# Kernel optimization log

Hardware: AMD Instinct MI355X
Metric: run time of the kernel (lower is better)

The kernel has to match this reference:

```python
import jax, jax.numpy as jnp
import numpy as np
import math

A = 32; B = 32; PSIZE = 16; K = 3; STRIDE = 2; PAD = 1; ITERS = 3; FINAL_LAMBDA = 0.01
KK = K * K; KKA = KK * A; KKA2 = KKA // 2 + 1
EPS = 1e-12; LN2PI = math.log(2 * math.pi)


def unfold(x, k, s, p):
    # torch F.unfold: output feature dim ordered (C, kh, kw), columns row-major
    b, C, h, w = x.shape
    xp = jnp.pad(x, ((0, 0), (0, 0), (p, p), (p, p)))
    oh = (h + 2 * p - k) // s + 1
    ow = (w + 2 * p - k) // s + 1
    cols = [xp[:, :, ki:ki + s * (oh - 1) + 1:s, kj:kj + s * (ow - 1) + 1:s]
            for ki in range(k) for kj in range(k)]
    patches = jnp.stack(cols, axis=2)  # [b, C, kk, oh, ow]
    return patches.reshape(b, C, k * k, oh * ow), oh, ow


def setup_inputs():
    key = jax.random.key(0)
    ks = jax.random.split(key, 8)
    b, h, w = 4, 14, 14
    a_in = jax.random.uniform(ks[0], (b, A, h, w), dtype=jnp.float32)
    pose = jax.random.normal(ks[1], (b, A * PSIZE, h, w), dtype=jnp.float32)
    mpose_w = jax.random.normal(ks[2], (B * PSIZE, PSIZE), dtype=jnp.float32) / np.float32(np.sqrt(PSIZE))
    mpose_b = jnp.zeros((B * PSIZE,), jnp.float32)
    freq_w = jax.random.normal(ks[3], (KKA2, PSIZE, 2), dtype=jnp.float32) * 0.02
    ln_g = jnp.ones((A,), jnp.float32)
    ln_b = jnp.zeros((A,), jnp.float32)
    lim = np.float32(np.sqrt(6.0 / (KK + KK)))  # xavier_uniform on [kk, kk, 1]
    spat_w = jax.random.uniform(ks[4], (KK, KK, 1), jnp.float32, -lim, lim)
    spat_bias = jnp.ones((KK,), jnp.float32)
    beta_u = jnp.zeros((1, 1, B, 1), jnp.float32)
    beta_a = jnp.zeros((1, 1, B), jnp.float32)
    return dict(a_in=a_in, pose=pose, mpose_w=mpose_w, mpose_b=mpose_b,
                freq_w=freq_w, ln_g=ln_g, ln_b=ln_b, spat_w=spat_w,
                spat_bias=spat_bias, beta_u=beta_u, beta_a=beta_a)


def _forward(a_in, pose, mpose_w, mpose_b, freq_w, ln_g, ln_b,
             spat_w, spat_bias, beta_u, beta_a):
    b = a_in.shape[0]
    pose_u, oh, ow = unfold(pose, K, STRIDE, PAD)  # [b, A*PSIZE, KK, l]
    l = oh * ow
    pose_u = pose_u.reshape(b, A, PSIZE, KK, l)
    pose_u = pose_u.transpose(0, 4, 3, 1, 2).reshape(b, l, KKA, PSIZE)
    # mpose linear: psize -> B*psize
    po = jnp.einsum('blkp,qp->blkq', pose_u, mpose_w) + mpose_b
    po = po.reshape(b * l, KKA, B, PSIZE)
    # Frequency FFT filter over kkA axis (weight shared across all B slices)
    xf = jnp.fft.rfft(po, axis=1, norm='ortho')        # [bl, KKA2, B, PSIZE] complex
    wc = freq_w[..., 0] + 1j * freq_w[..., 1]           # [KKA2, PSIZE]
    xf = xf * wc[None, :, None, :]
    po = jnp.fft.irfft(xf, n=KKA, axis=1, norm='ortho') + po  # residual
    v = po.reshape(b, l, KKA, B, PSIZE)
    a_u, _, _ = unfold(a_in, K, STRIDE, PAD)            # [b, A, KK, l]
    a_u = a_u.transpose(0, 3, 2, 1).reshape(b, l, KKA)
    # Spatial gating applied to ones-initialized r (identical for every B slice)
    ones = jnp.ones((b * l, KKA), jnp.float32)
    g = ones.reshape(b * l, KK, A)
    mu_g = g.mean(-1, keepdims=True)
    var_g = ((g - mu_g) ** 2).mean(-1, keepdims=True)
    gn = (g - mu_g) / jnp.sqrt(var_g + 1e-5) * ln_g + ln_b
    g2 = jnp.einsum('ij,nja->nia', spat_w[:, :, 0], gn) + spat_bias[None, :, None]
    gate = jax.nn.gelu(g2, approximate=False).reshape(b * l, KKA) + ones
    logit = jnp.broadcast_to(gate[:, :, None], (b * l, KKA, B))
    r = jax.nn.softmax(logit, axis=2).reshape(b, l, KKA, B, 1)
    a_out = mu = None
    for i in range(ITERS):
        lam = FINAL_LAMBDA * (1.0 - 0.95 ** (i + 1))
        # m-step
        rr = r * a_u[:, :, :, None, None]
        r_sum = rr.sum(axis=2, keepdims=True)                 # [b,l,1,B,1]
        coeff = rr / (r_sum + EPS)
        mu = (coeff * v).sum(axis=2, keepdims=True)           # [b,l,1,B,PSIZE]
        sig = (coeff * (v - mu) ** 2).sum(axis=2, keepdims=True) + EPS
        cost = (beta_u + jnp.log(jnp.sqrt(sig[:, :, 0]))) * r_sum[:, :, 0]  # [b,l,B,PSIZE]
        a_out = jax.nn.sigmoid(lam * (beta_a - cost.sum(axis=3)))           # [b,l,B]
        if i < ITERS - 1:
            # e-step (note: log(sigma_sq * ln2pi) is faithful to the original code)
            ln_p = (-0.5 * jnp.sum(jnp.log(sig * LN2PI), axis=-1)
                    - jnp.sum((v - mu) ** 2 / (2.0 * sig), axis=-1))        # [b,l,KKA,B]
            ln_ap = ln_p + jnp.log(a_out[:, :, None, :])
            r = jax.nn.softmax(ln_ap, axis=-1)[..., None]
    pose_out = mu[:, :, 0].reshape(b, l, B * PSIZE).transpose(0, 2, 1).reshape(b, B * PSIZE, oh, ow)
    a_fin = a_out.transpose(0, 2, 1).reshape(b, B, oh, ow)
    return a_fin, pose_out


def reference(a_in, pose, mpose_w, mpose_b, freq_w, ln_g, ln_b,
              spat_w, spat_bias, beta_u, beta_a):
    return _forward(a_in, pose, mpose_w, mpose_b, freq_w, ln_g, ln_b,
                    spat_w, spat_bias, beta_u, beta_a)
```

## Files before the change

kernel.cpp:

```cpp
#include <hip/hip_runtime.h>
#include <hip/hip_bf16.h>
#include <math.h>

#define A_    32
#define B_    32
#define PS    16
#define KK_   9
#define KKA_  288
#define OH_   7
#define L_    49
#define NB    4
#define NSITE 196

#define LAM1 5.0e-4f
#define LAM2 9.75e-4f
#define LAM3 1.42625e-3f
#define LOG_LN2PI 0.6086775903077413f

typedef _Float16 half2v __attribute__((ext_vector_type(2)));
typedef _Float16 half4v __attribute__((ext_vector_type(4)));
typedef short    short8 __attribute__((ext_vector_type(8)));
typedef float    floatx4 __attribute__((ext_vector_type(4)));

static __device__ __forceinline__ float san(float x, float lo, float hi){
    return fminf(fmaxf(x, lo), hi);
}

static __device__ __forceinline__ float dot2acc(half2v a, half2v b, float c){
#if __has_builtin(__builtin_amdgcn_fdot2)
    return __builtin_amdgcn_fdot2(a, b, c, false);
#else
    return c + (float)a.x*(float)b.x + (float)a.y*(float)b.y;
#endif
}

__global__ void k_prep_c(const float* __restrict__ fw,
                         ushort* __restrict__ cpr, float* __restrict__ csum)
{
    int id = blockIdx.x*256 + threadIdx.x;
    if (id >= 16*288) return;
    int p = id / 288, m = id % 288;
    float acc = fw[(0*16 + p)*2 + 0];
    for (int k = 1; k <= 143; ++k){
        float re = fw[(k*16 + p)*2 + 0];
        float im = fw[(k*16 + p)*2 + 1];
        int km = (k*m) % 288;
        float ang = 0.021816615649929116f * (float)km;
        float s, c; sincosf(ang, &s, &c);
        acc += 2.0f*(re*c - im*s);
    }
    float re144 = fw[(144*16 + p)*2 + 0];
    acc += re144 * ((m & 1) ? -1.0f : 1.0f);
    float cv = acc * (1.0f/288.0f);
    if (m == 0) cv += 1.0f;
    cv = san(cv, -1e4f, 1e4f);

    __hip_bfloat16 hb = __float2bfloat16(cv);
    float hif = __bfloat162float(hb);
    __hip_bfloat16 lb = __float2bfloat16(cv - hif);
    ushort hi = *(ushort*)&hb, lo = *(ushort*)&lb;

    ushort* c0h = cpr + p*592;
    ushort* c1h = cpr + 16*592   + p*592;
    ushort* c0l = cpr + 16*592*2 + p*592;
    ushort* c1l = cpr + 16*592*3 + p*592;
    int x1 = 288 - m;
    c0h[x1] = hi;  c0l[x1] = lo;
    c1h[x1-1] = hi; c1l[x1-1] = lo;
    if (m >= 1){
        int x2 = 576 - m;
        c0h[x2] = hi;  c0l[x2] = lo;
        c1h[x2-1] = hi; c1l[x2-1] = lo;
    } else {
        c0h[0] = hi; c0l[0] = lo;
        csum[p] = san(1.0f + fw[(0*16 + p)*2 + 0], -1e4f, 1e4f);
    }
}

__global__ void k_prep_x(const float* __restrict__ pose,
                         __hip_bfloat16* __restrict__ Xt, int n0, int cols)
{
    int id = blockIdx.x*256 + threadIdx.x;
    if (id >= cols*KKA_) return;
    int c = id / KKA_, j = id % KKA_;
    int n = n0 + (c >> 4), q = c & 15;
    int bs = n / L_, l = n % L_, oy = l / OH_, ox = l % OH_;
    int kk = j >> 5, a = j & 31;
    int y = oy*2 - 1 + kk/3, x = ox*2 - 1 + kk%3;
    float v = 0.f;
    if ((unsigned)y < 14u && (unsigned)x < 14u)
        v = pose[((bs*(A_*PS) + a*PS + q)*14 + y)*14 + x];
    Xt[id] = __float2bfloat16(san(v, -1e4f, 1e4f));
}

__launch_bounds__(256)
__global__ void k_stageB(const ushort* __restrict__ cpr, const __hip_bfloat16* __restrict__ Xt,
                         _Float16* __restrict__ U, int cols, int ns)
{
    const int bx = blockIdx.x, by = blockIdx.y, p = blockIdx.z;
    const int t = threadIdx.x;
    const int w = t >> 6, lane = t & 63;
    const int mn = lane & 15, quad = lane >> 4;
    const int i0 = by*48;
    const int col = bx*64 + w*16 + mn;
    const int colc = (col < cols) ? col : (cols - 1);

    const ushort* c0h = cpr + p*592;
    const ushort* c1h = cpr + 16*592   + p*592;
    const ushort* c0l = cpr + 16*592*2 + p*592;
    const ushort* c1l = cpr + 16*592*3 + p*592;

    floatx4 acc[3] = {{0,0,0,0},{0,0,0,0},{0,0,0,0}};
    for (int k0 = 0; k0 < 288; k0 += 32){
        short8 bfrag = *(const short8*)&Xt[colc*KKA_ + k0 + quad*8];
        #pragma unroll
        for (int s = 0; s < 3; ++s){
            int o = 288 + k0 + quad*8 - (i0 + s*16 + mn);
            int sel = o & 1;
            int off = o - sel;
            const ushort* bh = sel ? c1h : c0h;
            const ushort* bl = sel ? c1l : c0l;
            short8 ah = *(const short8*)&bh[off];
            short8 al = *(const short8*)&bl[off];
            acc[s] = __builtin_amdgcn_mfma_f32_16x16x32_bf16(ah, bfrag, acc[s], 0, 0, 0);
            acc[s] = __builtin_amdgcn_mfma_f32_16x16x32_bf16(al, bfrag, acc[s], 0, 0, 0);
        }
    }
    if (col < cols){
        const int nn = col >> 4, q0 = col & 15;
        #pragma unroll
        for (int s = 0; s < 3; ++s){
            #pragma unroll
            for (int r = 0; r < 4; ++r){
                int i = i0 + s*16 + quad*4 + r;
                U[(i*ns + nn)*256 + p*16 + q0] = (_Float16)acc[s][r];
            }
        }
    }
}

__launch_bounds__(512, 2)
__global__ void
k_em(const _Float16* __restrict__ U, const float* __restrict__ a_in,
     const float* __restrict__ mpw, const float* __restrict__ mpb,
     const float* __restrict__ csum,
     const float* __restrict__ beta_u, const float* __restrict__ beta_a,
     int n0, int ns, float* __restrict__ out)
{
    const int nl = blockIdx.x;
    const int n  = n0 + nl;
    const int t = threadIdx.x;
    const int Bc = t >> 4, p = t & 15;
    const int bs = n / L_, l = n % L_;

    __shared__ uint  v_lds[72][512];
    __shared__ float a_s[KKA_];
    __shared__ float d_s[16][33];
    __shared__ float rbuf[16][33];
    __shared__ float cst[32];

    for (int j = t; j < KKA_; j += 512){
        int kk = j >> 5, a = j & 31;
        int oy = l / OH_, ox = l % OH_;
        int y = oy*2 - 1 + kk/3, x = ox*2 - 1 + kk%3;
        float v = 0.f;
        if ((unsigned)y < 14u && (unsigned)x < 14u)
            v = a_in[((bs*A_ + a)*14 + y)*14 + x];
        a_s[j] = san(v, 0.f, 1e4f);
    }
    half2v w_h[8];
    #pragma unroll
    for (int k = 0; k < 8; ++k){
        w_h[k].x = (_Float16)mpw[t*16 + 2*k];
        w_h[k].y = (_Float16)mpw[t*16 + 2*k + 1];
    }
    const float vb = mpb[t] * csum[p];
    const float bu = beta_u[Bc];
    const float ba = beta_a[Bc];
    __syncthreads();

    float S0tot = 0.f;
    for (int j = 0; j < KKA_; ++j) S0tot += a_s[j];

    const _Float16* Up = U + nl*256 + p*16;
    const int istr = ns*256;

    half2v v_h[72];
    float S1 = 0.f, S2 = 0.f;
    for (int ch = 0; ch < 9; ++ch){
        #pragma unroll
        for (int k = 0; k < 8; ++k){
            const int i0 = ch*16 + 2*k;
            union { uint4 u4; half2v h2[4]; } A0, A1, B0, B1;
            A0.u4 = *(const uint4*)&Up[i0*istr];
            A1.u4 = *(const uint4*)&Up[i0*istr + 8];
            B0.u4 = *(const uint4*)&Up[(i0+1)*istr];
            B1.u4 = *(const uint4*)&Up[(i0+1)*istr + 8];
            float v0 = vb, v1 = vb;
            #pragma unroll
            for (int m = 0; m < 4; ++m){
                v0 = dot2acc(A0.h2[m], w_h[m],   v0);
                v0 = dot2acc(A1.h2[m], w_h[4+m], v0);
                v1 = dot2acc(B0.h2[m], w_h[m],   v1);
                v1 = dot2acc(B1.h2[m], w_h[4+m], v1);
            }
            const float a0 = a_s[i0], a1 = a_s[i0+1];
            S1 += a0*v0 + a1*v1;
            S2 += a0*v0*v0 + a1*v1*v1;
            union { half2v h; uint u; } cv;
            cv.h.x = (_Float16)v0; cv.h.y = (_Float16)v1;
            v_lds[ch*8 + k][t] = cv.u;
        }
    }
    #pragma unroll
    for (int ch = 0; ch < 9; ++ch){
        #pragma unroll
        for (int k = 0; k < 8; ++k){
            const int i0 = 144 + ch*16 + 2*k;
            union { uint4 u4; half2v h2[4]; } A0, A1, B0, B1;
            A0.u4 = *(const uint4*)&Up[i0*istr];
            A1.u4 = *(const uint4*)&Up[i0*istr + 8];
            B0.u4 = *(const uint4*)&Up[(i0+1)*istr];
            B1.u4 = *(const uint4*)&Up[(i0+1)*istr + 8];
            float v0 = vb, v1 = vb;
            #pragma unroll
            for (int m = 0; m < 4; ++m){
                v0 = dot2acc(A0.h2[m], w_h[m],   v0);
                v0 = dot2acc(A1.h2[m], w_h[4+m], v0);
                v1 = dot2acc(B0.h2[m], w_h[m],   v1);
                v1 = dot2acc(B1.h2[m], w_h[4+m], v1);
            }
            const float a0 = a_s[i0], a1 = a_s[i0+1];
            S1 += a0*v0 + a1*v1;
            S2 += a0*v0*v0 + a1*v1*v1;
            half2v vh; vh.x = (_Float16)v0; vh.y = (_Float16)v1;
            v_h[ch*8 + k] = vh;
        }
    }

    float mu_r, i2s_r;
    {
        const float rs  = S0tot * (1.0f/32.0f);
        const float inv = 1.0f / (rs + 1e-12f);
        const float S1r = S1 * (1.0f/32.0f), S2r = S2 * (1.0f/32.0f);
        mu_r = S1r * inv;
        const float sg  = fmaxf((S2r - 2.f*mu_r*S1r + mu_r*mu_r*rs) * inv, 0.f) + 1e-12f;
        i2s_r = 0.5f / sg;
        const float lg  = logf(sg);
        float cs = (bu + 0.5f*lg) * rs;
        float ls = lg + LOG_LN2PI;
        #pragma unroll
        for (int m = 1; m < 16; m <<= 1){ cs += __shfl_xor(cs, m, 16); ls += __shfl_xor(ls, m, 16); }
        const float aout = san(1.f/(1.f + expf(-LAM1*(ba - cs))), 1e-30f, 1.f);
        if (p == 0) cst[Bc] = logf(aout) - 0.5f*ls;
    }
    __syncthreads();

    const int b0 = p & 1, b1 = (p>>1)&1, b2 = (p>>2)&1, b3 = (p>>3)&1;
    float muF = 0.f, aF = 0.f;
    for (int it = 0; it < 2; ++it){
        const float lam = it ? LAM3 : LAM2;
        float T0 = 0.f, T1 = 0.f, T2 = 0.f;

        auto process = [&](int ibase, auto getpair){
            float e1[8], e2[4], e3[2], dfin;
            #pragma unroll
            for (int s = 0; s < 8; ++s){
                float v0, v1; getpair(s, v0, v1);
                float d0 = v0 - mu_r, d1 = v1 - mu_r;
                float ea = d0*d0*i2s_r, eb = d1*d1*i2s_r;
                float aown  = b0 ? eb : ea;
                float asend = b0 ? ea : eb;
                e1[s] = aown + __shfl_xor(asend, 1);
            }
            #pragma unroll
            for (int s = 0; s < 4; ++s){
                float aown  = b1 ? e1[2*s+1] : e1[2*s];
                float asend = b1 ? e1[2*s]   : e1[2*s+1];
                e2[s] = aown + __shfl_xor(asend, 2);
            }
            #pragma unroll
            for (int s = 0; s < 2; ++s){
                float aown  = b2 ? e2[2*s+1] : e2[2*s];
                float asend = b2 ? e2[2*s]   : e2[2*s+1];
                e3[s] = aown + __shfl_xor(asend, 4);
            }
            {
                float aown  = b3 ? e3[1] : e3[0];
                float asend = b3 ? e3[0] : e3[1];
                dfin = aown + __shfl_xor(asend, 8);
            }
            d_s[p][Bc] = dfin;
            __syncthreads();
            {
                const int isub = t >> 5, Bce = t & 31;
                float lnap = cst[Bce] - d_s[isub][Bce];
                float mx = lnap;
                #pragma unroll
                for (int m = 16; m >= 1; m >>= 1) mx = fmaxf(mx, __shfl_xor(mx, m));
                float ex = expf(lnap - mx);
                float sm = ex;
                #pragma unroll
                for (int m = 16; m >= 1; m >>= 1) sm += __shfl_xor(sm, m);
                rbuf[isub][Bce] = (ex / sm) * a_s[ibase + isub];
            }
            __syncthreads();
            #pragma unroll
            for (int s = 0; s < 8; ++s){
                float v0, v1; getpair(s, v0, v1);
                float r0 = rbuf[2*s][Bc], r1 = rbuf[2*s+1][Bc];
                T0 += r0 + r1;
                T1 += r0*v0 + r1*v1;
                T2 += r0*v0*v0 + r1*v1*v1;
            }
        };

        for (int ch = 0; ch < 9; ++ch){
            process(ch*16, [&](int s, float& v0, float& v1){
                union { uint u; half2v h; } cv; cv.u = v_lds[ch*8 + s][t];
                v0 = (float)cv.h.x; v1 = (float)cv.h.y;
            });
        }
        #pragma unroll
        for (int ch = 0; ch < 9; ++ch){
            process(144 + ch*16, [&](int s, float& v0, float& v1){
                half2v vh = v_h[ch*8 + s];
                v0 = (float)vh.x; v1 = (float)vh.y;
            });
        }

        const float inv = 1.f/(T0 + 1e-12f);
        const float mu  = T1 * inv;
        const float sg  = fmaxf((T2 - 2.f*mu*T1 + mu*mu*T0) * inv, 0.f) + 1e-12f;
        const float lg  = logf(sg);
        float cs = (bu + 0.5f*lg) * T0;
        float ls = lg + LOG_LN2PI;
        #pragma unroll
        for (int m = 1; m < 16; m <<= 1){ cs += __shfl_xor(cs, m, 16); ls += __shfl_xor(ls, m, 16); }
        const float aout = san(1.f/(1.f + expf(-lam*(ba - cs))), 1e-30f, 1.f);
        if (it == 0){
            mu_r = mu; i2s_r = 0.5f/sg;
            if (p == 0) cst[Bc] = logf(aout) - 0.5f*ls;
            __syncthreads();
        } else { muF = mu; aF = aout; }
    }

    if (p == 0) out[bs*(B_*L_) + Bc*L_ + l] = san(aF, 0.f, 1.f);
    out[6272 + (bs*512 + t)*L_ + l] = san(muF, -1e4f, 1e4f);
}

extern "C" void kernel_launch(void* const* d_in, const int* in_sizes, int n_in,
                              void* d_out, int out_size, void* d_ws, size_t ws_size,
                              hipStream_t stream)
{
    const float* a_in   = (const float*)d_in[0];
    const float* pose   = (const float*)d_in[1];
    const float* mpw    = (const float*)d_in[2];
    const float* mpb    = (const float*)d_in[3];
    const float* fw     = (const float*)d_in[4];
    const float* beta_u = (const float*)d_in[9];
    const float* beta_a = (const float*)d_in[10];
    float* out = (float*)d_out;

    char* base = (char*)d_ws;
    float*  csum = (float*)(base + 0);
    ushort* cpr  = (ushort*)(base + 256);

    const int opts[] = {196, 98, 49, 28, 14, 7, 4, 2, 1};
    int ns = 1;
    for (int oi = 0; oi < 9; ++oi){
        size_t need = 76288u + (size_t)156672u * (size_t)opts[oi];
        if (need <= ws_size){ ns = opts[oi]; break; }
    }
    const int G = NSITE / ns;
    const int cols = ns * PS;
    __hip_bfloat16* Xt = (__hip_bfloat16*)(base + 76288);
    _Float16*       Ug = (_Float16*)(base + 76288 + (size_t)9216*ns);

    k_prep_c<<<18, 256, 0, stream>>>(fw, cpr, csum);
    for (int g = 0; g < G; ++g){
        const int n0 = g * ns;
        k_prep_x<<<(cols*KKA_ + 255)/256, 256, 0, stream>>>(pose, Xt, n0, cols);
        k_stageB<<<dim3((cols + 63)/64, 6, 16), 256, 0, stream>>>(cpr, Xt, Ug, cols, ns);
        k_em    <<<ns, 512, 0, stream>>>(Ug, a_in, mpw, mpb, csum, beta_u, beta_a, n0, ns, out);
    }
}
```

Baseline: 285.8 us.

## Merge prep kernels, reorder EM register loads, cap k_em VGPRs

The two preparation kernels are fused into one launch, with extra blocks computing the filter coefficients on the first group, which removes one kernel launch. In k_em, the register-resident half of the transformed poses is now computed first in an unrolled loop with scheduling barriers, followed by the LDS-resident half. An amdgpu_num_vgpr(224) attribute is added to constrain register use. This aims to cut launch overhead and control register pressure and instruction scheduling, but the VGPR cap and sched barriers risk spills or reduced latency hiding.

```diff
diff --git a/kernel.cpp b/kernel.cpp
--- a/kernel.cpp
+++ b/kernel.cpp
@@ -22,6 +22,16 @@
 typedef short    short8 __attribute__((ext_vector_type(8)));
 typedef float    floatx4 __attribute__((ext_vector_type(4)));
 
+#if defined(__has_attribute)
+#  if __has_attribute(amdgpu_num_vgpr)
+#    define KEM_VGPR_ATTR __attribute__((amdgpu_num_vgpr(224)))
+#  else
+#    define KEM_VGPR_ATTR
+#  endif
+#else
+#  define KEM_VGPR_ATTR
+#endif
+
 static __device__ __forceinline__ float san(float x, float lo, float hi){
     return fminf(fmaxf(x, lo), hi);
 }
@@ -34,52 +44,59 @@
 #endif
 }
 
-__global__ void k_prep_c(const float* __restrict__ fw,
-                         ushort* __restrict__ cpr, float* __restrict__ csum)
+static __device__ __forceinline__ void sched_fence(){
+#if __has_builtin(__builtin_amdgcn_sched_barrier)
+    __builtin_amdgcn_sched_barrier(0);
+#else
+    asm volatile("" ::: "memory");
+#endif
+}
+
+__global__ void k_prep(const float* __restrict__ fw, const float* __restrict__ pose,
+                       ushort* __restrict__ cpr, float* __restrict__ csum,
+                       __hip_bfloat16* __restrict__ Xt, int n0, int cols, int nx)
 {
-    int id = blockIdx.x*256 + threadIdx.x;
-    if (id >= 16*288) return;
-    int p = id / 288, m = id % 288;
-    float acc = fw[(0*16 + p)*2 + 0];
-    for (int k = 1; k <= 143; ++k){
-        float re = fw[(k*16 + p)*2 + 0];
-        float im = fw[(k*16 + p)*2 + 1];
-        int km = (k*m) % 288;
-        float ang = 0.021816615649929116f * (float)km;
-        float s, c; sincosf(ang, &s, &c);
-        acc += 2.0f*(re*c - im*s);
-    }
-    float re144 = fw[(144*16 + p)*2 + 0];
-    acc += re144 * ((m & 1) ? -1.0f : 1.0f);
-    float cv = acc * (1.0f/288.0f);
-    if (m == 0) cv += 1.0f;
-    cv = san(cv, -1e4f, 1e4f);
-
-    __hip_bfloat16 hb = __float2bfloat16(cv);
-    float hif = __bfloat162float(hb);
-    __hip_bfloat16 lb = __float2bfloat16(cv - hif);
-    ushort hi = *(ushort*)&hb, lo = *(ushort*)&lb;
-
-    ushort* c0h = cpr + p*592;
-    ushort* c1h = cpr + 16*592   + p*592;
-    ushort* c0l = cpr + 16*592*2 + p*592;
-    ushort* c1l = cpr + 16*592*3 + p*592;
-    int x1 = 288 - m;
-    c0h[x1] = hi;  c0l[x1] = lo;
-    c1h[x1-1] = hi; c1l[x1-1] = lo;
-    if (m >= 1){
-        int x2 = 576 - m;
-        c0h[x2] = hi;  c0l[x2] = lo;
-        c1h[x2-1] = hi; c1l[x2-1] = lo;
-    } else {
-        c0h[0] = hi; c0l[0] = lo;
-        csum[p] = san(1.0f + fw[(0*16 + p)*2 + 0], -1e4f, 1e4f);
-    }
-}
-
-__global__ void k_prep_x(const float* __restrict__ pose,
-                         __hip_bfloat16* __restrict__ Xt, int n0, int cols)
-{
+    if ((int)blockIdx.x >= nx){
+        int id = ((int)blockIdx.x - nx)*256 + threadIdx.x;
+        if (id >= 16*288) return;
+        int p = id / 288, m = id % 288;
+        float acc = fw[(0*16 + p)*2 + 0];
+        for (int k = 1; k <= 143; ++k){
+            float re = fw[(k*16 + p)*2 + 0];
+            float im = fw[(k*16 + p)*2 + 1];
+            int km = (k*m) % 288;
+            float ang = 0.021816615649929116f * (float)km;
+            float s, c; sincosf(ang, &s, &c);
+            acc += 2.0f*(re*c - im*s);
+        }
+        float re144 = fw[(144*16 + p)*2 + 0];
+        acc += re144 * ((m & 1) ? -1.0f : 1.0f);
+        float cv = acc * (1.0f/288.0f);
+        if (m == 0) cv += 1.0f;
+        cv = san(cv, -1e4f, 1e4f);
+
+        __hip_bfloat16 hb = __float2bfloat16(cv);
+        float hif = __bfloat162float(hb);
+        __hip_bfloat16 lb = __float2bfloat16(cv - hif);
+        ushort hi = *(ushort*)&hb, lo = *(ushort*)&lb;
+
+        ushort* c0h = cpr + p*592;
+        ushort* c1h = cpr + 16*592   + p*592;
+        ushort* c0l = cpr + 16*592*2 + p*592;
+        ushort* c1l = cpr + 16*592*3 + p*592;
+        int x1 = 288 - m;
+        c0h[x1] = hi;  c0l[x1] = lo;
+        c1h[x1-1] = hi; c1l[x1-1] = lo;
+        if (m >= 1){
+            int x2 = 576 - m;
+            c0h[x2] = hi;  c0l[x2] = lo;
+            c1h[x2-1] = hi; c1l[x2-1] = lo;
+        } else {
+            c0h[0] = hi; c0l[0] = lo;
+            csum[p] = san(1.0f + fw[(0*16 + p)*2 + 0], -1e4f, 1e4f);
+        }
+        return;
+    }
     int id = blockIdx.x*256 + threadIdx.x;
     if (id >= cols*KKA_) return;
     int c = id / KKA_, j = id % KKA_;
@@ -139,7 +156,7 @@
     }
 }
 
-__launch_bounds__(512, 2)
+__launch_bounds__(512, 2) KEM_VGPR_ATTR
 __global__ void
 k_em(const _Float16* __restrict__ U, const float* __restrict__ a_in,
      const float* __restrict__ mpw, const float* __restrict__ mpb,
@@ -185,8 +202,37 @@
     const _Float16* Up = U + nl*256 + p*16;
     const int istr = ns*256;
 
+    float S1 = 0.f, S2 = 0.f;
+
     half2v v_h[72];
-    float S1 = 0.f, S2 = 0.f;
+    #pragma unroll
+    for (int g = 0; g < 36; ++g){
+        #pragma unroll
+        for (int k2 = 0; k2 < 2; ++k2){
+            const int pr = g*2 + k2;
+            const int i0 = 144 + pr*2;
+            union { uint4 u4; half2v h2[4]; } A0, A1, B0, B1;
+            A0.u4 = *(const uint4*)&Up[i0*istr];
+            A1.u4 = *(const uint4*)&Up[i0*istr + 8];
+            B0.u4 = *(const uint4*)&Up[(i0+1)*istr];
+            B1.u4 = *(const uint4*)&Up[(i0+1)*istr + 8];
+            float v0 = vb, v1 = vb;
+            #pragma unroll
+            for (int m = 0; m < 4; ++m){
+                v0 = dot2acc(A0.h2[m], w_h[m],   v0);
+                v0 = dot2acc(A1.h2[m], w_h[4+m], v0);
+                v1 = dot2acc(B0.h2[m], w_h[m],   v1);
+                v1 = dot2acc(B1.h2[m], w_h[4+m], v1);
+            }
+            const float a0 = a_s[i0], a1 = a_s[i0+1];
+            S1 += a0*v0 + a1*v1;
+            S2 += a0*v0*v0 + a1*v1*v1;
+            half2v vh; vh.x = (_Float16)v0; vh.y = (_Float16)v1;
+            v_h[pr] = vh;
+        }
+        sched_fence();
+    }
+
     for (int ch = 0; ch < 9; ++ch){
         #pragma unroll
         for (int k = 0; k < 8; ++k){
@@ -210,31 +256,6 @@
             union { half2v h; uint u; } cv;
             cv.h.x = (_Float16)v0; cv.h.y = (_Float16)v1;
             v_lds[ch*8 + k][t] = cv.u;
-        }
-    }
-    #pragma unroll
-    for (int ch = 0; ch < 9; ++ch){
-        #pragma unroll
-        for (int k = 0; k < 8; ++k){
-            const int i0 = 144 + ch*16 + 2*k;
-            union { uint4 u4; half2v h2[4]; } A0, A1, B0, B1;
-            A0.u4 = *(const uint4*)&Up[i0*istr];
-            A1.u4 = *(const uint4*)&Up[i0*istr + 8];
-            B0.u4 = *(const uint4*)&Up[(i0+1)*istr];
-            B1.u4 = *(const uint4*)&Up[(i0+1)*istr + 8];
-            float v0 = vb, v1 = vb;
-            #pragma unroll
-            for (int m = 0; m < 4; ++m){
-                v0 = dot2acc(A0.h2[m], w_h[m],   v0);
-                v0 = dot2acc(A1.h2[m], w_h[4+m], v0);
-                v1 = dot2acc(B0.h2[m], w_h[m],   v1);
-                v1 = dot2acc(B1.h2[m], w_h[4+m], v1);
-            }
-            const float a0 = a_s[i0], a1 = a_s[i0+1];
-            S1 += a0*v0 + a1*v1;
-            S2 += a0*v0*v0 + a1*v1*v1;
-            half2v vh; vh.x = (_Float16)v0; vh.y = (_Float16)v1;
-            v_h[ch*8 + k] = vh;
         }
     }
 
@@ -377,10 +398,11 @@
     __hip_bfloat16* Xt = (__hip_bfloat16*)(base + 76288);
     _Float16*       Ug = (_Float16*)(base + 76288 + (size_t)9216*ns);
 
-    k_prep_c<<<18, 256, 0, stream>>>(fw, cpr, csum);
     for (int g = 0; g < G; ++g){
         const int n0 = g * ns;
-        k_prep_x<<<(cols*KKA_ + 255)/256, 256, 0, stream>>>(pose, Xt, n0, cols);
+        const int nx = (cols*KKA_ + 255)/256;
+        const int nc = (g == 0) ? 18 : 0;
+        k_prep  <<<nx + nc, 256, 0, stream>>>(fw, pose, cpr, csum, Xt, n0, cols, nx);
         k_stageB<<<dim3((cols + 63)/64, 6, 16), 256, 0, stream>>>(cpr, Xt, Ug, cols, ns);
         k_em    <<<ns, 512, 0, stream>>>(Ug, a_in, mpw, mpb, csum, beta_u, beta_a, n0, ns, out);
     }
```

After: 281.1 us. Within noise of the previous version (-1.7%).

## Fuse circulant MFMA stage into EM kernel and merge prep kernels

Applied to the files above, without the earlier changes.

Merges the filter-coefficient and patch-gather prep kernels into one launch. Folds the circulant-filter MFMA stage into the EM kernel, so each site block computes its own filtered pose chunk into shared memory instead of writing U to global memory and reading it back. It also removes the chunked multi-launch loop over sites and switches sincosf to the fast intrinsic. The cost is extra shared memory, per-chunk __syncthreads, lower occupancy (launch bounds 512,1), and possibly slower coefficient precision.

```diff
diff --git a/kernel.cpp b/kernel.cpp
--- a/kernel.cpp
+++ b/kernel.cpp
@@ -11,6 +11,7 @@
 #define L_    49
 #define NB    4
 #define NSITE 196
+#define NCOLS 3136
 
 #define LAM1 5.0e-4f
 #define LAM2 9.75e-4f
@@ -18,7 +19,6 @@
 #define LOG_LN2PI 0.6086775903077413f
 
 typedef _Float16 half2v __attribute__((ext_vector_type(2)));
-typedef _Float16 half4v __attribute__((ext_vector_type(4)));
 typedef short    short8 __attribute__((ext_vector_type(8)));
 typedef float    floatx4 __attribute__((ext_vector_type(4)));
 
@@ -34,56 +34,55 @@
 #endif
 }
 
-__global__ void k_prep_c(const float* __restrict__ fw,
-                         ushort* __restrict__ cpr, float* __restrict__ csum)
+__global__ void k_prep(const float* __restrict__ fw, const float* __restrict__ pose,
+                       ushort* __restrict__ cpr, float* __restrict__ csum,
+                       __hip_bfloat16* __restrict__ Xt, int nc)
 {
-    int id = blockIdx.x*256 + threadIdx.x;
-    if (id >= 16*288) return;
-    int p = id / 288, m = id % 288;
-    float acc = fw[(0*16 + p)*2 + 0];
-    for (int k = 1; k <= 143; ++k){
-        float re = fw[(k*16 + p)*2 + 0];
-        float im = fw[(k*16 + p)*2 + 1];
-        int km = (k*m) % 288;
-        float ang = 0.021816615649929116f * (float)km;
-        float s, c; sincosf(ang, &s, &c);
-        acc += 2.0f*(re*c - im*s);
-    }
-    float re144 = fw[(144*16 + p)*2 + 0];
-    acc += re144 * ((m & 1) ? -1.0f : 1.0f);
-    float cv = acc * (1.0f/288.0f);
-    if (m == 0) cv += 1.0f;
-    cv = san(cv, -1e4f, 1e4f);
-
-    __hip_bfloat16 hb = __float2bfloat16(cv);
-    float hif = __bfloat162float(hb);
-    __hip_bfloat16 lb = __float2bfloat16(cv - hif);
-    ushort hi = *(ushort*)&hb, lo = *(ushort*)&lb;
-
-    ushort* c0h = cpr + p*592;
-    ushort* c1h = cpr + 16*592   + p*592;
-    ushort* c0l = cpr + 16*592*2 + p*592;
-    ushort* c1l = cpr + 16*592*3 + p*592;
-    int x1 = 288 - m;
-    c0h[x1] = hi;  c0l[x1] = lo;
-    c1h[x1-1] = hi; c1l[x1-1] = lo;
-    if (m >= 1){
-        int x2 = 576 - m;
-        c0h[x2] = hi;  c0l[x2] = lo;
-        c1h[x2-1] = hi; c1l[x2-1] = lo;
-    } else {
-        c0h[0] = hi; c0l[0] = lo;
-        csum[p] = san(1.0f + fw[(0*16 + p)*2 + 0], -1e4f, 1e4f);
-    }
-}
-
-__global__ void k_prep_x(const float* __restrict__ pose,
-                         __hip_bfloat16* __restrict__ Xt, int n0, int cols)
-{
-    int id = blockIdx.x*256 + threadIdx.x;
-    if (id >= cols*KKA_) return;
+    if ((int)blockIdx.x < nc){
+        int id = (int)blockIdx.x*256 + threadIdx.x;
+        if (id >= 16*288) return;
+        int p = id / 288, m = id % 288;
+        float acc = fw[(0*16 + p)*2 + 0];
+        for (int k = 1; k <= 143; ++k){
+            float re = fw[(k*16 + p)*2 + 0];
+            float im = fw[(k*16 + p)*2 + 1];
+            int km = (k*m) % 288;
+            float ang = 0.021816615649929116f * (float)km;
+            float s, c; __sincosf(ang, &s, &c);
+            acc += 2.0f*(re*c - im*s);
+        }
+        float re144 = fw[(144*16 + p)*2 + 0];
+        acc += re144 * ((m & 1) ? -1.0f : 1.0f);
+        float cv = acc * (1.0f/288.0f);
+        if (m == 0) cv += 1.0f;
+        cv = san(cv, -1e4f, 1e4f);
+
+        __hip_bfloat16 hb = __float2bfloat16(cv);
+        float hif = __bfloat162float(hb);
+        __hip_bfloat16 lb = __float2bfloat16(cv - hif);
+        ushort hi = *(ushort*)&hb, lo = *(ushort*)&lb;
+
+        ushort* c0h = cpr + p*592;
+        ushort* c1h = cpr + 16*592   + p*592;
+        ushort* c0l = cpr + 16*592*2 + p*592;
+        ushort* c1l = cpr + 16*592*3 + p*592;
+        int x1 = 288 - m;
+        c0h[x1] = hi;  c0l[x1] = lo;
+        c1h[x1-1] = hi; c1l[x1-1] = lo;
+        if (m >= 1){
+            int x2 = 576 - m;
+            c0h[x2] = hi;  c0l[x2] = lo;
+            c1h[x2-1] = hi; c1l[x2-1] = lo;
+        } else {
+            c0h[0] = hi; c0l[0] = lo;
+            csum[p] = san(1.0f + fw[(0*16 + p)*2 + 0], -1e4f, 1e4f);
+        }
+        return;
+    }
+    int id = ((int)blockIdx.x - nc)*256 + threadIdx.x;
+    if (id >= NCOLS*KKA_) return;
     int c = id / KKA_, j = id % KKA_;
-    int n = n0 + (c >> 4), q = c & 15;
+    int n = c >> 4, q = c & 15;
     int bs = n / L_, l = n % L_, oy = l / OH_, ox = l % OH_;
     int kk = j >> 5, a = j & 31;
     int y = oy*2 - 1 + kk/3, x = ox*2 - 1 + kk%3;
@@ -93,71 +92,26 @@
     Xt[id] = __float2bfloat16(san(v, -1e4f, 1e4f));
 }
 
-__launch_bounds__(256)
-__global__ void k_stageB(const ushort* __restrict__ cpr, const __hip_bfloat16* __restrict__ Xt,
-                         _Float16* __restrict__ U, int cols, int ns)
-{
-    const int bx = blockIdx.x, by = blockIdx.y, p = blockIdx.z;
-    const int t = threadIdx.x;
-    const int w = t >> 6, lane = t & 63;
-    const int mn = lane & 15, quad = lane >> 4;
-    const int i0 = by*48;
-    const int col = bx*64 + w*16 + mn;
-    const int colc = (col < cols) ? col : (cols - 1);
-
-    const ushort* c0h = cpr + p*592;
-    const ushort* c1h = cpr + 16*592   + p*592;
-    const ushort* c0l = cpr + 16*592*2 + p*592;
-    const ushort* c1l = cpr + 16*592*3 + p*592;
-
-    floatx4 acc[3] = {{0,0,0,0},{0,0,0,0},{0,0,0,0}};
-    for (int k0 = 0; k0 < 288; k0 += 32){
-        short8 bfrag = *(const short8*)&Xt[colc*KKA_ + k0 + quad*8];
-        #pragma unroll
-        for (int s = 0; s < 3; ++s){
-            int o = 288 + k0 + quad*8 - (i0 + s*16 + mn);
-            int sel = o & 1;
-            int off = o - sel;
-            const ushort* bh = sel ? c1h : c0h;
-            const ushort* bl = sel ? c1l : c0l;
-            short8 ah = *(const short8*)&bh[off];
-            short8 al = *(const short8*)&bl[off];
-            acc[s] = __builtin_amdgcn_mfma_f32_16x16x32_bf16(ah, bfrag, acc[s], 0, 0, 0);
-            acc[s] = __builtin_amdgcn_mfma_f32_16x16x32_bf16(al, bfrag, acc[s], 0, 0, 0);
-        }
-    }
-    if (col < cols){
-        const int nn = col >> 4, q0 = col & 15;
-        #pragma unroll
-        for (int s = 0; s < 3; ++s){
-            #pragma unroll
-            for (int r = 0; r < 4; ++r){
-                int i = i0 + s*16 + quad*4 + r;
-                U[(i*ns + nn)*256 + p*16 + q0] = (_Float16)acc[s][r];
-            }
-        }
-    }
-}
-
-__launch_bounds__(512, 2)
+__launch_bounds__(512, 1)
 __global__ void
-k_em(const _Float16* __restrict__ U, const float* __restrict__ a_in,
-     const float* __restrict__ mpw, const float* __restrict__ mpb,
-     const float* __restrict__ csum,
-     const float* __restrict__ beta_u, const float* __restrict__ beta_a,
-     int n0, int ns, float* __restrict__ out)
+k_mega(const ushort* __restrict__ cpr, const __hip_bfloat16* __restrict__ Xt,
+       const float* __restrict__ a_in,
+       const float* __restrict__ mpw, const float* __restrict__ mpb,
+       const float* __restrict__ csum,
+       const float* __restrict__ beta_u, const float* __restrict__ beta_a,
+       float* __restrict__ out)
 {
     const int nl = blockIdx.x;
-    const int n  = n0 + nl;
     const int t = threadIdx.x;
     const int Bc = t >> 4, p = t & 15;
-    const int bs = n / L_, l = n % L_;
-
-    __shared__ uint  v_lds[72][512];
-    __shared__ float a_s[KKA_];
-    __shared__ float d_s[16][33];
-    __shared__ float rbuf[16][33];
-    __shared__ float cst[32];
+    const int bs = nl / L_, l = nl % L_;
+
+    __shared__ uint      v_lds[72][512];
+    __shared__ _Float16  us[16*264];
+    __shared__ float     a_s[KKA_];
+    __shared__ float     d_s[16][33];
+    __shared__ float     rbuf[16][33];
+    __shared__ float     cst[32];
 
     for (int j = t; j < KKA_; j += 512){
         int kk = j >> 5, a = j & 31;
@@ -182,20 +136,49 @@
     float S0tot = 0.f;
     for (int j = 0; j < KKA_; ++j) S0tot += a_s[j];
 
-    const _Float16* Up = U + nl*256 + p*16;
-    const int istr = ns*256;
-
+    const int w = t >> 6, lane = t & 63;
+    const int mn = lane & 15, quad = lane >> 4;
+    const int p0 = w*2;
+    const __hip_bfloat16* xrow = Xt + (nl*16 + mn)*KKA_ + quad*8;
+
+    float S1 = 0.f, S2 = 0.f;
     half2v v_h[72];
-    float S1 = 0.f, S2 = 0.f;
+
     for (int ch = 0; ch < 9; ++ch){
-        #pragma unroll
-        for (int k = 0; k < 8; ++k){
-            const int i0 = ch*16 + 2*k;
+        floatx4 accA = {0,0,0,0}, accB = {0,0,0,0};
+        for (int k0i = 0; k0i < 9; ++k0i){
+            const int k0 = k0i*32;
+            short8 bfrag = *(const short8*)&xrow[k0];
+            #pragma unroll
+            for (int pp = 0; pp < 2; ++pp){
+                const int pg = p0 + pp;
+                int o = 288 + k0 + quad*8 - (ch*16 + mn);
+                int sel = o & 1, off = o - sel;
+                const ushort* bh = cpr + (sel ? 16*592 : 0) + pg*592;
+                const ushort* bl = cpr + 16*592*2 + (sel ? 16*592 : 0) + pg*592;
+                short8 ah = *(const short8*)&bh[off];
+                short8 al = *(const short8*)&bl[off];
+                floatx4 acc = pp ? accB : accA;
+                acc = __builtin_amdgcn_mfma_f32_16x16x32_bf16(ah, bfrag, acc, 0, 0, 0);
+                acc = __builtin_amdgcn_mfma_f32_16x16x32_bf16(al, bfrag, acc, 0, 0, 0);
+                if (pp) accB = acc; else accA = acc;
+            }
+        }
+        #pragma unroll
+        for (int r = 0; r < 4; ++r){
+            us[p0*264     + (quad*4 + r)*16 + mn] = (_Float16)accA[r];
+            us[(p0+1)*264 + (quad*4 + r)*16 + mn] = (_Float16)accB[r];
+        }
+        __syncthreads();
+        const _Float16* urow = &us[p*264];
+        #pragma unroll
+        for (int s = 0; s < 8; ++s){
+            const int i0 = ch*16 + 2*s;
             union { uint4 u4; half2v h2[4]; } A0, A1, B0, B1;
-            A0.u4 = *(const uint4*)&Up[i0*istr];
-            A1.u4 = *(const uint4*)&Up[i0*istr + 8];
-            B0.u4 = *(const uint4*)&Up[(i0+1)*istr];
-            B1.u4 = *(const uint4*)&Up[(i0+1)*istr + 8];
+            A0.u4 = *(const uint4*)&urow[(2*s)*16];
+            A1.u4 = *(const uint4*)&urow[(2*s)*16 + 8];
+            B0.u4 = *(const uint4*)&urow[(2*s+1)*16];
+            B1.u4 = *(const uint4*)&urow[(2*s+1)*16 + 8];
             float v0 = vb, v1 = vb;
             #pragma unroll
             for (int m = 0; m < 4; ++m){
@@ -209,19 +192,47 @@
             S2 += a0*v0*v0 + a1*v1*v1;
             union { half2v h; uint u; } cv;
             cv.h.x = (_Float16)v0; cv.h.y = (_Float16)v1;
-            v_lds[ch*8 + k][t] = cv.u;
-        }
+            v_lds[ch*8 + s][t] = cv.u;
+        }
+        __syncthreads();
     }
     #pragma unroll
-    for (int ch = 0; ch < 9; ++ch){
-        #pragma unroll
-        for (int k = 0; k < 8; ++k){
-            const int i0 = 144 + ch*16 + 2*k;
+    for (int c2 = 0; c2 < 9; ++c2){
+        const int ch = 9 + c2;
+        floatx4 accA = {0,0,0,0}, accB = {0,0,0,0};
+        for (int k0i = 0; k0i < 9; ++k0i){
+            const int k0 = k0i*32;
+            short8 bfrag = *(const short8*)&xrow[k0];
+            #pragma unroll
+            for (int pp = 0; pp < 2; ++pp){
+                const int pg = p0 + pp;
+                int o = 288 + k0 + quad*8 - (ch*16 + mn);
+                int sel = o & 1, off = o - sel;
+                const ushort* bh = cpr + (sel ? 16*592 : 0) + pg*592;
+                const ushort* bl = cpr + 16*592*2 + (sel ? 16*592 : 0) + pg*592;
+                short8 ah = *(const short8*)&bh[off];
+                short8 al = *(const short8*)&bl[off];
+                floatx4 acc = pp ? accB : accA;
+                acc = __builtin_amdgcn_mfma_f32_16x16x32_bf16(ah, bfrag, acc, 0, 0, 0);
+                acc = __builtin_amdgcn_mfma_f32_16x16x32_bf16(al, bfrag, acc, 0, 0, 0);
+                if (pp) accB = acc; else accA = acc;
+            }
+        }
+        #pragma unroll
+        for (int r = 0; r < 4; ++r){
+            us[p0*264     + (quad*4 + r)*16 + mn] = (_Float16)accA[r];
+            us[(p0+1)*264 + (quad*4 + r)*16 + mn] = (_Float16)accB[r];
+        }
+        __syncthreads();
+        const _Float16* urow = &us[p*264];
+        #pragma unroll
+        for (int s = 0; s < 8; ++s){
+            const int i0 = ch*16 + 2*s;
             union { uint4 u4; half2v h2[4]; } A0, A1, B0, B1;
-            A0.u4 = *(const uint4*)&Up[i0*istr];
-            A1.u4 = *(const uint4*)&Up[i0*istr + 8];
-            B0.u4 = *(const uint4*)&Up[(i0+1)*istr];
-            B1.u4 = *(const uint4*)&Up[(i0+1)*istr + 8];
+            A0.u4 = *(const uint4*)&urow[(2*s)*16];
+            A1.u4 = *(const uint4*)&urow[(2*s)*16 + 8];
+            B0.u4 = *(const uint4*)&urow[(2*s+1)*16];
+            B1.u4 = *(const uint4*)&urow[(2*s+1)*16 + 8];
             float v0 = vb, v1 = vb;
             #pragma unroll
             for (int m = 0; m < 4; ++m){
@@ -234,8 +245,9 @@
             S1 += a0*v0 + a1*v1;
             S2 += a0*v0*v0 + a1*v1*v1;
             half2v vh; vh.x = (_Float16)v0; vh.y = (_Float16)v1;
-            v_h[ch*8 + k] = vh;
-        }
+            v_h[c2*8 + s] = vh;
+        }
+        __syncthreads();
     }
 
     float mu_r, i2s_r;
@@ -365,23 +377,10 @@
     char* base = (char*)d_ws;
     float*  csum = (float*)(base + 0);
     ushort* cpr  = (ushort*)(base + 256);
-
-    const int opts[] = {196, 98, 49, 28, 14, 7, 4, 2, 1};
-    int ns = 1;
-    for (int oi = 0; oi < 9; ++oi){
-        size_t need = 76288u + (size_t)156672u * (size_t)opts[oi];
-        if (need <= ws_size){ ns = opts[oi]; break; }
-    }
-    const int G = NSITE / ns;
-    const int cols = ns * PS;
     __hip_bfloat16* Xt = (__hip_bfloat16*)(base + 76288);
-    _Float16*       Ug = (_Float16*)(base + 76288 + (size_t)9216*ns);
-
-    k_prep_c<<<18, 256, 0, stream>>>(fw, cpr, csum);
-    for (int g = 0; g < G; ++g){
-        const int n0 = g * ns;
-        k_prep_x<<<(cols*KKA_ + 255)/256, 256, 0, stream>>>(pose, Xt, n0, cols);
-        k_stageB<<<dim3((cols + 63)/64, 6, 16), 256, 0, stream>>>(cpr, Xt, Ug, cols, ns);
-        k_em    <<<ns, 512, 0, stream>>>(Ug, a_in, mpw, mpb, csum, beta_u, beta_a, n0, ns, out);
-    }
-}
+
+    const int nc = 18;
+    const int nx = (NCOLS*KKA_ + 255)/256;
+    k_prep<<<nc + nx, 256, 0, stream>>>(fw, pose, cpr, csum, Xt, nc);
+    k_mega<<<NSITE, 512, 0, stream>>>(cpr, Xt, a_in, mpw, mpb, csum, beta_u, beta_a, out);
+}
```

New measurement: 252.7 us. -11.6%, faster.
